# Performance work log

Measured on AMD Instinct MI355X. Metric: run time of the kernel, lower is better.

Reference implementation:

```python
import jax, jax.numpy as jnp
import numpy as np

N = 512
N_B = 32
N_C = 16
NUM_CH = 20


def setup_inputs() -> dict:
    key = jax.random.key(0)
    ks = jax.random.split(key, 9)
    x = jax.random.normal(ks[0], (N, NUM_CH), dtype=jnp.float32)
    # fc1: 20 -> 128
    W1 = jax.random.normal(ks[1], (NUM_CH, 128), dtype=jnp.float32) * (1.0 / np.sqrt(NUM_CH))
    b1 = jnp.zeros((128,), dtype=jnp.float32)
    # fc2: 128 -> 20
    W2 = jax.random.normal(ks[2], (128, NUM_CH), dtype=jnp.float32) * (1.0 / np.sqrt(128))
    b2 = jnp.zeros((NUM_CH,), dtype=jnp.float32)
    # minibatch-discrimination tensor T: (20, n_B*n_C)
    T = jax.random.normal(ks[3], (NUM_CH, N_B * N_C), dtype=jnp.float32) * 0.1
    # fc3: (20 + n_B) -> 1
    W3 = jax.random.normal(ks[4], (NUM_CH + N_B, 1), dtype=jnp.float32) * (1.0 / np.sqrt(NUM_CH + N_B))
    b3 = jnp.zeros((1,), dtype=jnp.float32)
    return {"x": x, "W1": W1, "b1": b1, "W2": W2, "b2": b2, "T": T, "W3": W3, "b3": b3}


def reference(x, W1, b1, W2, b2, T, W3, b3):
    h = jax.nn.relu(x @ W1 + b1)            # (N, 128)
    h = jax.nn.relu(h @ W2 + b2)            # (N, 20)
    M = (h @ T).reshape(-1, N_B, N_C)       # (N, n_B, n_C)
    # pairwise L1 distance over n_C: (N, n_B, n_C, 1) - (1, n_B, n_C, N)
    d = jnp.sum(jnp.abs(M[:, :, :, None] - jnp.transpose(M, (1, 2, 0))[None]), axis=2)  # (N, n_B, N)
    o = jnp.sum(jnp.exp(-d), axis=2)        # (N, n_B)
    o = o - jnp.mean(o)
    feat = jnp.concatenate([h, o], axis=1)  # (N, 20 + n_B)
    return jax.nn.sigmoid(feat @ W3 + b3)   # (N, 1)
```

## Files before the change

### kernel.cpp

```cpp
#include <hip/hip_runtime.h>
#include <math.h>

#define N 512
#define NB 32
#define NC 16
#define CH 20
#define JP 4
#define NUNITS (32 * 8 * JP)

#define WS_H 0
#define WS_M 10240
#define WS_S 272384
#define WS_OSUM 272896
#define WS_CNT 272928

__global__ __launch_bounds__(128) void k1_fwd(
        const float* __restrict__ x,
        const float* __restrict__ W1, const float* __restrict__ b1,
        const float* __restrict__ W2, const float* __restrict__ b2,
        const float* __restrict__ T,
        float* __restrict__ h_g, float* __restrict__ M_g,
        float* __restrict__ s_g, float* __restrict__ osum32,
        int* __restrict__ counter)
{
    const int i = blockIdx.x;
    const int t = threadIdx.x;
    __shared__ float xs[CH];
    __shared__ float h1s[128];
    __shared__ float hs[CH];

    if (t == 0) s_g[i] = 0.f;
    if (i == 0) {
        if (t < NB) osum32[t] = 0.f;
        if (t == 0) *counter = 0;
    }
    if (t < CH) xs[t] = x[i * CH + t];
    __syncthreads();

    float a = b1[t];
    #pragma unroll
    for (int k = 0; k < CH; ++k) a += xs[k] * W1[k * 128 + t];
    h1s[t] = fmaxf(a, 0.f);
    __syncthreads();

    if (t < CH) {
        float a2 = b2[t];
        #pragma unroll 16
        for (int k = 0; k < 128; ++k) a2 += h1s[k] * W2[k * CH + t];
        a2 = fmaxf(a2, 0.f);
        hs[t] = a2;
        h_g[i * CH + t] = a2;
    }
    __syncthreads();

    #pragma unroll
    for (int r = 0; r < 4; ++r) {
        const int m = t + r * 128;
        float a3 = 0.f;
        #pragma unroll
        for (int k = 0; k < CH; ++k) a3 += hs[k] * T[k * N + m];
        M_g[i * N + m] = a3;
    }
}

__global__ __launch_bounds__(256) void k2_odist(
        const float* __restrict__ M_g, const float* __restrict__ h_g,
        const float* __restrict__ W3, const float* __restrict__ b3,
        float* __restrict__ s_g, float* __restrict__ osum32,
        int* __restrict__ counter, float* __restrict__ out)
{
    const int t = threadIdx.x;
    const int unit = blockIdx.x;
    const int b  = unit & 31;
    const int ic = (unit >> 5) & 7;
    const int jp = unit >> 8;

    __shared__ __align__(16) float sj[128][NC];
    __shared__ float red[4][64];
    __shared__ int last;
    __shared__ float smean;

    {
        const int row = t >> 1, half = t & 1;
        const float4* src = reinterpret_cast<const float4*>(
            M_g + (size_t)(jp * 128 + row) * N + b * NC + half * 8);
        float4 v0 = src[0], v1 = src[1];
        float4* dst = reinterpret_cast<float4*>(&sj[row][half * 8]);
        dst[0] = v0; dst[1] = v1;
    }

    const int lane = t & 63;
    const int w = t >> 6;
    const int i = ic * 64 + lane;
    float mi[NC];
    {
        const float4* src = reinterpret_cast<const float4*>(M_g + (size_t)i * N + b * NC);
        float4 a0 = src[0], a1 = src[1], a2 = src[2], a3 = src[3];
        mi[0]=a0.x; mi[1]=a0.y; mi[2]=a0.z; mi[3]=a0.w;
        mi[4]=a1.x; mi[5]=a1.y; mi[6]=a1.z; mi[7]=a1.w;
        mi[8]=a2.x; mi[9]=a2.y; mi[10]=a2.z; mi[11]=a2.w;
        mi[12]=a3.x; mi[13]=a3.y; mi[14]=a3.z; mi[15]=a3.w;
    }
    __syncthreads();

    float acc = 0.f;
    #pragma unroll 4
    for (int jl = 0; jl < 32; ++jl) {
        const float4* s4v = reinterpret_cast<const float4*>(sj[w * 32 + jl]);
        const float4 s0 = s4v[0], s1 = s4v[1], s2 = s4v[2], s3 = s4v[3];
        float d0 = fabsf(mi[0]  - s0.x) + fabsf(mi[4]  - s1.x)
                 + fabsf(mi[8]  - s2.x) + fabsf(mi[12] - s3.x);
        float d1 = fabsf(mi[1]  - s0.y) + fabsf(mi[5]  - s1.y)
                 + fabsf(mi[9]  - s2.y) + fabsf(mi[13] - s3.y);
        float d2 = fabsf(mi[2]  - s0.z) + fabsf(mi[6]  - s1.z)
                 + fabsf(mi[10] - s2.z) + fabsf(mi[14] - s3.z);
        float d3 = fabsf(mi[3]  - s0.w) + fabsf(mi[7]  - s1.w)
                 + fabsf(mi[11] - s2.w) + fabsf(mi[15] - s3.w);
        acc += __expf(-((d0 + d1) + (d2 + d3)));
    }

    red[w][lane] = acc;
    __syncthreads();
    if (t < 64) {
        const float s4 = red[0][t] + red[1][t] + red[2][t] + red[3][t];
        atomicAdd(&s_g[ic * 64 + t], s4 * W3[CH + b]);
        float v = s4;
        #pragma unroll
        for (int off = 32; off > 0; off >>= 1) v += __shfl_down(v, off, 64);
        if (t == 0) atomicAdd(&osum32[b], v);
    }

    asm volatile("s_waitcnt vmcnt(0)" ::: "memory");
    if (t == 0) {
        const int old = atomicAdd(counter, 1);
        last = (old == NUNITS - 1) ? 1 : 0;
    }
    __syncthreads();
    if (!last) return;

    float v = 0.f;
    if (t < NB) v = atomicAdd(&osum32[t], 0.f);
    if (t < 64) {
        #pragma unroll
        for (int off = 16; off > 0; off >>= 1) v += __shfl_down(v, off, 64);
        if (t == 0) smean = v * (1.f / (float)(N * NB));
    }
    __syncthreads();
    const float mean = smean;

    float w3sum = 0.f;
    #pragma unroll
    for (int bb = 0; bb < NB; ++bb) w3sum += W3[CH + bb];

    #pragma unroll
    for (int r = 0; r < 2; ++r) {
        const int ii = t + r * 256;
        const float sv = atomicAdd(&s_g[ii], 0.f);
        float a = b3[0] + sv - mean * w3sum;
        #pragma unroll
        for (int k = 0; k < CH; ++k) a += h_g[ii * CH + k] * W3[k];
        out[ii] = 1.f / (1.f + __expf(-a));
    }
}

extern "C" void kernel_launch(void* const* d_in, const int* in_sizes, int n_in,
                              void* d_out, int out_size, void* d_ws, size_t ws_size,
                              hipStream_t stream) {
    const float* x  = (const float*)d_in[0];
    const float* W1 = (const float*)d_in[1];
    const float* b1 = (const float*)d_in[2];
    const float* W2 = (const float*)d_in[3];
    const float* b2 = (const float*)d_in[4];
    const float* T  = (const float*)d_in[5];
    const float* W3 = (const float*)d_in[6];
    const float* b3 = (const float*)d_in[7];
    float* out = (float*)d_out;

    float* ws     = (float*)d_ws;
    float* h_g    = ws + WS_H;
    float* M_g    = ws + WS_M;
    float* s_g    = ws + WS_S;
    float* osum32 = ws + WS_OSUM;
    int*   counter = (int*)(ws + WS_CNT);

    k1_fwd<<<N, 128, 0, stream>>>(x, W1, b1, W2, b2, T, h_g, M_g, s_g, osum32, counter);
    k2_odist<<<NUNITS, 256, 0, stream>>>(M_g, h_g, W3, b3, s_g, osum32, counter, out);
}
```

Measured before the change: 93.06 us.

## Replace last-block atomic counter finalize with separate final kernel

Moves the h·W3 dot product and b3 into the first kernel, so h no longer has to be written to global memory and the finalize only needs s_g. The last-block detection (global counter atomic, vmcnt wait, atomic reads) is removed from the distance kernel and replaced by a third single-block kernel that computes the mean and sigmoid. This takes the counter atomic and memory fence off every distance block, at the cost of an extra kernel launch.

```diff
diff --git a/kernel.cpp b/kernel.cpp
--- a/kernel.cpp
+++ b/kernel.cpp
@@ -8,20 +8,18 @@
 #define JP 4
 #define NUNITS (32 * 8 * JP)
 
-#define WS_H 0
-#define WS_M 10240
-#define WS_S 272384
-#define WS_OSUM 272896
-#define WS_CNT 272928
+#define WS_M 0
+#define WS_S 262144
+#define WS_OSUM 262656
 
 __global__ __launch_bounds__(128) void k1_fwd(
         const float* __restrict__ x,
         const float* __restrict__ W1, const float* __restrict__ b1,
         const float* __restrict__ W2, const float* __restrict__ b2,
         const float* __restrict__ T,
-        float* __restrict__ h_g, float* __restrict__ M_g,
-        float* __restrict__ s_g, float* __restrict__ osum32,
-        int* __restrict__ counter)
+        const float* __restrict__ W3, const float* __restrict__ b3,
+        float* __restrict__ M_g, float* __restrict__ s_g,
+        float* __restrict__ osum32)
 {
     const int i = blockIdx.x;
     const int t = threadIdx.x;
@@ -29,11 +27,7 @@
     __shared__ float h1s[128];
     __shared__ float hs[CH];
 
-    if (t == 0) s_g[i] = 0.f;
-    if (i == 0) {
-        if (t < NB) osum32[t] = 0.f;
-        if (t == 0) *counter = 0;
-    }
+    if (i == 0 && t < NB) osum32[t] = 0.f;
     if (t < CH) xs[t] = x[i * CH + t];
     __syncthreads();
 
@@ -43,13 +37,20 @@
     h1s[t] = fmaxf(a, 0.f);
     __syncthreads();
 
+    float a2 = 0.f;
     if (t < CH) {
-        float a2 = b2[t];
+        a2 = b2[t];
         #pragma unroll 16
         for (int k = 0; k < 128; ++k) a2 += h1s[k] * W2[k * CH + t];
         a2 = fmaxf(a2, 0.f);
         hs[t] = a2;
-        h_g[i * CH + t] = a2;
+    }
+
+    if (t < 64) {
+        float p = (t < CH) ? a2 * W3[t] : 0.f;
+        #pragma unroll
+        for (int off = 32; off > 0; off >>= 1) p += __shfl_down(p, off, 64);
+        if (t == 0) s_g[i] = p + b3[0];
     }
     __syncthreads();
 
@@ -64,10 +65,8 @@
 }
 
 __global__ __launch_bounds__(256) void k2_odist(
-        const float* __restrict__ M_g, const float* __restrict__ h_g,
-        const float* __restrict__ W3, const float* __restrict__ b3,
-        float* __restrict__ s_g, float* __restrict__ osum32,
-        int* __restrict__ counter, float* __restrict__ out)
+        const float* __restrict__ M_g, const float* __restrict__ W3,
+        float* __restrict__ s_g, float* __restrict__ osum32)
 {
     const int t = threadIdx.x;
     const int unit = blockIdx.x;
@@ -77,8 +76,6 @@
 
     __shared__ __align__(16) float sj[128][NC];
     __shared__ float red[4][64];
-    __shared__ int last;
-    __shared__ float smean;
 
     {
         const int row = t >> 1, half = t & 1;
@@ -129,38 +126,29 @@
         for (int off = 32; off > 0; off >>= 1) v += __shfl_down(v, off, 64);
         if (t == 0) atomicAdd(&osum32[b], v);
     }
+}
 
-    asm volatile("s_waitcnt vmcnt(0)" ::: "memory");
-    if (t == 0) {
-        const int old = atomicAdd(counter, 1);
-        last = (old == NUNITS - 1) ? 1 : 0;
-    }
-    __syncthreads();
-    if (!last) return;
+__global__ __launch_bounds__(512) void k3_final(
+        const float* __restrict__ s_g, const float* __restrict__ osum32,
+        const float* __restrict__ W3, float* __restrict__ out)
+{
+    const int t = threadIdx.x;
+    __shared__ float smean;
 
-    float v = 0.f;
-    if (t < NB) v = atomicAdd(&osum32[t], 0.f);
     if (t < 64) {
+        float v = (t < NB) ? osum32[t] : 0.f;
         #pragma unroll
-        for (int off = 16; off > 0; off >>= 1) v += __shfl_down(v, off, 64);
+        for (int off = 32; off > 0; off >>= 1) v += __shfl_down(v, off, 64);
         if (t == 0) smean = v * (1.f / (float)(N * NB));
     }
     __syncthreads();
-    const float mean = smean;
 
     float w3sum = 0.f;
     #pragma unroll
-    for (int bb = 0; bb < NB; ++bb) w3sum += W3[CH + bb];
+    for (int b = 0; b < NB; ++b) w3sum += W3[CH + b];
 
-    #pragma unroll
-    for (int r = 0; r < 2; ++r) {
-        const int ii = t + r * 256;
-        const float sv = atomicAdd(&s_g[ii], 0.f);
-        float a = b3[0] + sv - mean * w3sum;
-        #pragma unroll
-        for (int k = 0; k < CH; ++k) a += h_g[ii * CH + k] * W3[k];
-        out[ii] = 1.f / (1.f + __expf(-a));
-    }
+    const float a = s_g[t] - smean * w3sum;
+    out[t] = 1.f / (1.f + __expf(-a));
 }
 
 extern "C" void kernel_launch(void* const* d_in, const int* in_sizes, int n_in,
@@ -177,12 +165,11 @@
     float* out = (float*)d_out;
 
     float* ws     = (float*)d_ws;
-    float* h_g    = ws + WS_H;
     float* M_g    = ws + WS_M;
     float* s_g    = ws + WS_S;
     float* osum32 = ws + WS_OSUM;
-    int*   counter = (int*)(ws + WS_CNT);
 
-    k1_fwd<<<N, 128, 0, stream>>>(x, W1, b1, W2, b2, T, h_g, M_g, s_g, osum32, counter);
-    k2_odist<<<NUNITS, 256, 0, stream>>>(M_g, h_g, W3, b3, s_g, osum32, counter, out);
+    k1_fwd<<<N, 128, 0, stream>>>(x, W1, b1, W2, b2, T, W3, b3, M_g, s_g, osum32);
+    k2_odist<<<NUNITS, 256, 0, stream>>>(M_g, W3, s_g, osum32);
+    k3_final<<<1, 512, 0, stream>>>(s_g, osum32, W3, out);
 }
```

Measured after the change: 85.53 us. 1.09x faster.
